# Kernel tuning notes

Hardware: AMD Instinct MI355X
Metric: run time of the kernel (lower is better)

## Reference

```python
import jax, jax.numpy as jnp
import numpy as np


def setup_inputs() -> dict:
    key = jax.random.key(0)
    k1, k2, k3, k4 = jax.random.split(key, 4)
    B, C, L = 16, 512, 4096
    x = jax.random.normal(k1, (B, C, L), dtype=jnp.float32)
    # conv1d kernel_size=1, bias=False -> weight [3C, C]
    w_qkv = jax.random.normal(k2, (3 * C, C), dtype=jnp.float32) * (1.0 / np.sqrt(C))
    w_out = jax.random.normal(k3, (C, C), dtype=jnp.float32) * (1.0 / np.sqrt(C))
    b_out = jax.random.normal(k4, (C,), dtype=jnp.float32) * 0.01
    return {"x": x, "w_qkv": w_qkv, "w_out": w_out, "b_out": b_out}


def reference(x, w_qkv, w_out, b_out):
    # x: [b, c, l]; 1x1 conv == channel-wise matmul
    qkv = jnp.einsum('bcl,oc->bol', x, w_qkv)          # [b, 3c, l]
    q, k, v = jnp.split(qkv, 3, axis=1)                 # each [b, c, l] (heads=1)
    k = jax.nn.softmax(k, axis=-1)                      # softmax over sequence dim l
    context = jnp.einsum('bdn,ben->bde', k, v)          # [b, c, c]
    out = jnp.einsum('bde,bdn->ben', context, q)        # [b, c, l]
    return jnp.einsum('bcl,oc->bol', out, w_out) + b_out[None, :, None]
```

## Files before the change

### kernel.cpp

```cpp
#include <hip/hip_runtime.h>
#include <hip/hip_bf16.h>
#include <type_traits>

#define DEVINL __device__ __forceinline__

typedef float f32x4 __attribute__((ext_vector_type(4)));
typedef __bf16 bf16x8 __attribute__((ext_vector_type(8)));

DEVINL float bf2f(short s) {
  unsigned u = ((unsigned)(unsigned short)s) << 16;
  float f; __builtin_memcpy(&f, &u, 4); return f;
}
DEVINL short f2bf(float f) {
  unsigned u; __builtin_memcpy(&u, &f, 4);
  u += 0x7fff + ((u >> 16) & 1);
  return (short)(u >> 16);
}

DEVINL void gl_lds16(const void* g, void* l) {
  __builtin_amdgcn_global_load_lds(
      (const __attribute__((address_space(1))) void*)g,
      (__attribute__((address_space(3))) void*)l, 16, 0, 0);
}

DEVINL void swz_blk(int& bx, int& by, int& bz) {
  const int gx = gridDim.x, gy = gridDim.y;
  const int tpz = gx * gy;
  const int nwg = tpz * gridDim.z;
  int fid = bx + gx * (by + gy * bz);
  fid = (fid & 7) * (nwg >> 3) + (fid >> 3);
  bz = fid / tpz;
  const int r = fid - bz * tpz;
  by = r % gy;
  bx = r / gy;
}


template <typename OutT, bool BIAS, bool EXP>
DEVINL void epilogue_store(f32x4 (&acc)[4][4], char* smem,
                           OutT* __restrict__ C, int ldc, int m0, int n0,
                           const float* __restrict__ bias,
                           float* __restrict__ rowsum, int t) {
  const int wave = t >> 6, lane = t & 63;
  const int quad = lane >> 4, l16 = lane & 15;
  const int arow = (wave >> 1) * 64, brow = (wave & 1) * 64;
  if constexpr (std::is_same<OutT, float>::value) {
    float* tile = (float*)smem;
#pragma unroll
    for (int rnd = 0; rnd < 2; ++rnd) {
      if ((arow >> 6) == rnd) {
#pragma unroll
        for (int mi = 0; mi < 4; ++mi)
#pragma unroll
          for (int ni = 0; ni < 4; ++ni) {
            const int col = brow + ni * 16 + l16;
#pragma unroll
            for (int r = 0; r < 4; ++r) {
              const int row = mi * 16 + quad * 4 + r;
              float v = acc[mi][ni][r];
              if (BIAS) v += bias[m0 + rnd * 64 + row];
              tile[row * 128 + col] = v;
            }
          }
      }
      __syncthreads();
#pragma unroll
      for (int i = 0; i < 8; ++i) {
        const int row = wave * 16 + i * 2 + (lane >> 5);
        const int cf  = (lane & 31) * 4;
        f32x4 v = *(f32x4*)&tile[row * 128 + cf];
        *(f32x4*)&C[(long)(m0 + rnd * 64 + row) * ldc + n0 + cf] = v;
      }
      __syncthreads();
    }
  } else {
    short* tile = (short*)smem;
#pragma unroll
    for (int mi = 0; mi < 4; ++mi)
#pragma unroll
      for (int r = 0; r < 4; ++r) {
        const int row = arow + mi * 16 + quad * 4 + r;
        float rs = 0.f;
#pragma unroll
        for (int ni = 0; ni < 4; ++ni) {
          const int col = brow + ni * 16 + l16;
          float v = acc[mi][ni][r];
          if (BIAS) v += bias[m0 + row];
          if (EXP) { v = __expf(v); rs += v; }
          tile[row * 128 + col] = f2bf(v);
        }
        if (EXP) {
          rs += __shfl_xor(rs, 1); rs += __shfl_xor(rs, 2);
          rs += __shfl_xor(rs, 4); rs += __shfl_xor(rs, 8);
          if (l16 == 0) atomicAdd(&rowsum[m0 + row], rs);
        }
      }
    __syncthreads();
#pragma unroll
    for (int i = 0; i < 8; ++i) {
      const int row = wave * 32 + i * 4 + (lane >> 4);
      const int cs  = l16 * 8;
      int4 v = *(int4*)&tile[row * 128 + cs];
      *(int4*)&C[(long)(m0 + row) * ldc + n0 + cs] = v;
    }
  }
}

#define GEMM_K_LOOP(A_, lda_, B_, ldb_, kbeg_, kend_)                        \
  {                                                                          \
    const int lrow = t >> 2;                                                 \
    const int lk8  = (t & 3) * 8;                                            \
    auto stage = [&](int buf, int k0) {                                      \
      _Pragma("unroll")                                                      \
      for (int s = 0; s < 2; ++s) {                                          \
        gl_lds16(A_ + (long)(m0 + s * 64 + lrow) * lda_ + k0 + lk8,          \
                 smem + buf * 16384 + s * 4096 + wave * 1024);               \
        gl_lds16(B_ + (long)(n0 + s * 64 + lrow) * ldb_ + k0 + lk8,          \
                 smem + buf * 16384 + 8192 + s * 4096 + wave * 1024);        \
      }                                                                      \
    };                                                                       \
    stage(0, kbeg_);                                                         \
    __syncthreads();                                                         \
    int cur = 0;                                                             \
    for (int k0 = kbeg_; k0 < kend_; k0 += 32) {                             \
      if (k0 + 32 < kend_) stage(cur ^ 1, k0 + 32);                          \
      const short* As = (const short*)(smem + cur * 16384);                  \
      const short* Bs = (const short*)(smem + cur * 16384 + 8192);           \
      bf16x8 af[4], bfr[4];                                                  \
      _Pragma("unroll")                                                      \
      for (int i = 0; i < 4; ++i)                                            \
        af[i] = *(const bf16x8*)&As[(arow + i * 16 + l16) * 32 + quad * 8];  \
      _Pragma("unroll")                                                      \
      for (int i = 0; i < 4; ++i)                                            \
        bfr[i] = *(const bf16x8*)&Bs[(brow + i * 16 + l16) * 32 + quad * 8]; \
      _Pragma("unroll")                                                      \
      for (int mi = 0; mi < 4; ++mi)                                         \
        _Pragma("unroll")                                                    \
        for (int ni = 0; ni < 4; ++ni)                                       \
          acc[mi][ni] = __builtin_amdgcn_mfma_f32_16x16x32_bf16(             \
              af[mi], bfr[ni], acc[mi][ni], 0, 0, 0);                        \
      __syncthreads();                                                       \
      cur ^= 1;                                                              \
    }                                                                        \
  }

template <typename OutT, bool BIAS, bool EXP>
__global__ __launch_bounds__(256, 4)
void gemm_nt(const short* __restrict__ A, long sA, int lda,
             const short* __restrict__ B, long sB, int ldb,
             OutT* __restrict__ C, long sC, int ldc,
             const float* __restrict__ bias, float* __restrict__ rowsum, int K)
{
  int bx = blockIdx.x, by = blockIdx.y, bz = blockIdx.z;
  swz_blk(bx, by, bz);

  A += (long)bz * sA;
  B += (long)bz * sB;
  C += (long)bz * sC;
  if (EXP) rowsum += (long)bz * 512;

  __shared__ char smem[32768];

  const int t    = threadIdx.x;
  const int wave = t >> 6, lane = t & 63;
  const int quad = lane >> 4, l16 = lane & 15;
  const int m0 = by * 128, n0 = bx * 128;
  const int arow = (wave >> 1) * 64, brow = (wave & 1) * 64;

  f32x4 acc[4][4];
#pragma unroll
  for (int i = 0; i < 4; ++i)
#pragma unroll
    for (int j = 0; j < 4; ++j) acc[i][j] = (f32x4){0.f, 0.f, 0.f, 0.f};

  GEMM_K_LOOP(A, lda, B, ldb, 0, K)

  epilogue_store<OutT, BIAS, EXP>(acc, smem, C, ldc, m0, n0, bias, rowsum, t);
}


template <typename OutT, bool BIAS, bool EXP>
DEVINL void epilogue_store_wide(f32x4 (&acc)[4][4], char* smem,
                                OutT* __restrict__ C, int ldc, int m0, int n0,
                                const float* __restrict__ bias,
                                float* __restrict__ rowsum, int t) {
  const int wave = t >> 6, lane = t & 63;
  const int quad = lane >> 4, l16 = lane & 15;
  const int arow = (wave >> 2) * 64, brow = (wave & 3) * 64;
  const int rn_w = brow >> 7;
  const int colb = brow & 64;
  if constexpr (std::is_same<OutT, float>::value) {
    float* tile = (float*)smem;
    const int rm_w = arow >> 6;
#pragma unroll
    for (int rm = 0; rm < 2; ++rm)
#pragma unroll
      for (int rn = 0; rn < 2; ++rn) {
        if (rm_w == rm && rn_w == rn) {
#pragma unroll
          for (int mi = 0; mi < 4; ++mi)
#pragma unroll
            for (int ni = 0; ni < 4; ++ni)
#pragma unroll
              for (int r = 0; r < 4; ++r) {
                const int row = mi * 16 + quad * 4 + r;
                float v = acc[mi][ni][r];
                if (BIAS) v += bias[m0 + rm * 64 + row];
                tile[row * 128 + colb + ni * 16 + l16] = v;
              }
        }
        __syncthreads();
#pragma unroll
        for (int i = 0; i < 4; ++i) {
          const int row = wave * 8 + i * 2 + (lane >> 5);
          const int cf  = (lane & 31) * 4;
          *(f32x4*)&C[(long)(m0 + rm * 64 + row) * ldc + n0 + rn * 128 + cf] =
              *(f32x4*)&tile[row * 128 + cf];
        }
        __syncthreads();
      }
  } else {
    if (EXP) {
#pragma unroll
      for (int mi = 0; mi < 4; ++mi)
#pragma unroll
        for (int r = 0; r < 4; ++r) {
          const int row = arow + mi * 16 + quad * 4 + r;
          float rs = 0.f;
#pragma unroll
          for (int ni = 0; ni < 4; ++ni) {
            float v = __expf(acc[mi][ni][r]);
            acc[mi][ni][r] = v; rs += v;
          }
          rs += __shfl_xor(rs, 1); rs += __shfl_xor(rs, 2);
          rs += __shfl_xor(rs, 4); rs += __shfl_xor(rs, 8);
          if (l16 == 0) atomicAdd(&rowsum[m0 + row], rs);
        }
    }
    short* tile = (short*)smem;
#pragma unroll
    for (int rn = 0; rn < 2; ++rn) {
      if (rn_w == rn) {
#pragma unroll
        for (int mi = 0; mi < 4; ++mi)
#pragma unroll
          for (int ni = 0; ni < 4; ++ni)
#pragma unroll
            for (int r = 0; r < 4; ++r) {
              const int row = arow + mi * 16 + quad * 4 + r;
              float v = acc[mi][ni][r];
              if (BIAS) v += bias[m0 + row];
              tile[row * 128 + colb + ni * 16 + l16] = f2bf(v);
            }
      }
      __syncthreads();
#pragma unroll
      for (int i = 0; i < 4; ++i) {
        const int row = wave * 16 + i * 4 + (lane >> 4);
        const int cs  = l16 * 8;
        *(int4*)&C[(long)(m0 + row) * ldc + n0 + rn * 128 + cs] =
            *(int4*)&tile[row * 128 + cs];
      }
      __syncthreads();
    }
  }
}

#define WIDE_K_LOOP(A_, lda_, B_, ldb_, kbeg_, kend_)                        \
  {                                                                          \
    const int lrow = t >> 2;                                     \
    const int lk8  = (t & 3) * 8;                                            \
    auto stage = [&](int buf, int k0) {                                      \
      gl_lds16(A_ + (long)(m0 + lrow) * lda_ + k0 + lk8,                     \
               smem + buf * 24576 + wave * 1024);                            \
      _Pragma("unroll")                                                      \
      for (int s = 0; s < 2; ++s)                                            \
        gl_lds16(B_ + (long)(n0 + s * 128 + lrow) * ldb_ + k0 + lk8,         \
                 smem + buf * 24576 + 8192 + s * 8192 + wave * 1024);        \
    };                                                                       \
    auto compute = [&](int buf) {                                            \
      const short* As = (const short*)(smem + buf * 24576);                  \
      const short* Bs = (const short*)(smem + buf * 24576 + 8192);           \
      bf16x8 af[4], bfr[4];                                                  \
      _Pragma("unroll")                                                      \
      for (int i = 0; i < 4; ++i)                                            \
        af[i] = *(const bf16x8*)&As[(arow + i * 16 + l16) * 32 + quad * 8];  \
      _Pragma("unroll")                                                      \
      for (int i = 0; i < 4; ++i)                                            \
        bfr[i] = *(const bf16x8*)&Bs[(brow + i * 16 + l16) * 32 + quad * 8]; \
      _Pragma("unroll")                                                      \
      for (int mi = 0; mi < 4; ++mi)                                         \
        _Pragma("unroll")                                                    \
        for (int ni = 0; ni < 4; ++ni)                                       \
          acc[mi][ni] = __builtin_amdgcn_mfma_f32_16x16x32_bf16(             \
              af[mi], bfr[ni], acc[mi][ni], 0, 0, 0);                        \
    };                                                                       \
    stage(0, kbeg_);                                                         \
    stage(1, kbeg_ + 32);                                                    \
    int cur = 0;                                                             \
    for (int k0 = kbeg_; k0 < kend_ - 32; k0 += 32) {                        \
      asm volatile("s_waitcnt vmcnt(3)" ::: "memory");                       \
      __builtin_amdgcn_s_barrier();                                          \
      __builtin_amdgcn_sched_barrier(0);                                     \
      if (k0 + 64 < kend_) {                                                 \
        int nb = cur + 2; if (nb >= 3) nb -= 3;                              \
        stage(nb, k0 + 64);                                                  \
      }                                                                      \
      compute(cur);                                                          \
      ++cur; if (cur == 3) cur = 0;                                          \
    }                                                                        \
    asm volatile("s_waitcnt vmcnt(0)" ::: "memory");                         \
    __builtin_amdgcn_s_barrier();                                            \
    __builtin_amdgcn_sched_barrier(0);                                       \
    compute(cur);                                                            \
    __syncthreads();                        \
  }

template <typename OutT, bool BIAS, bool EXP>
__global__ __launch_bounds__(512, 4)
void gemm_nt_wide(const short* __restrict__ A, long sA, int lda,
                  const short* __restrict__ B, long sB, int ldb,
                  OutT* __restrict__ C, long sC, int ldc,
                  const float* __restrict__ bias, float* __restrict__ rowsum,
                  int K)
{
  int bx = blockIdx.x, by = blockIdx.y, bz = blockIdx.z;
  swz_blk(bx, by, bz);

  A += (long)bz * sA;
  B += (long)bz * sB;
  C += (long)bz * sC;
  if (EXP) rowsum += (long)bz * 512;

  __shared__ char smem[73728];

  const int t    = threadIdx.x;
  const int wave = t >> 6, lane = t & 63;
  const int quad = lane >> 4, l16 = lane & 15;
  const int m0 = by * 128, n0 = bx * 256;
  const int arow = (wave >> 2) * 64, brow = (wave & 3) * 64;

  f32x4 acc[4][4];
#pragma unroll
  for (int i = 0; i < 4; ++i)
#pragma unroll
    for (int j = 0; j < 4; ++j) acc[i][j] = (f32x4){0.f, 0.f, 0.f, 0.f};

  WIDE_K_LOOP(A, lda, B, ldb, 0, K)

  epilogue_store_wide<OutT, BIAS, EXP>(acc, smem, C, ldc, m0, n0, bias,
                                       rowsum, t);
}

__global__ __launch_bounds__(512, 4)
void gemm_sk_wide(const short* __restrict__ Ab, const short* __restrict__ Bb,
                  float* __restrict__ Cp)
{
  int bx = blockIdx.x, by = blockIdx.y, bz = blockIdx.z;
  swz_blk(bx, by, bz);

  const int b = bz >> 1, s = bz & 1;
  const short* A = Ab + (long)b * 2097152;
  const short* B = Bb + (long)b * 2097152;
  float* C = Cp + (long)(s * 16 + b) * 262144;

  __shared__ char smem[73728];

  const int t    = threadIdx.x;
  const int wave = t >> 6, lane = t & 63;
  const int quad = lane >> 4, l16 = lane & 15;
  const int m0 = by * 128, n0 = bx * 256;
  const int arow = (wave >> 2) * 64, brow = (wave & 3) * 64;
  const int kbeg = s * 2048, kend = kbeg + 2048;

  f32x4 acc[4][4];
#pragma unroll
  for (int i = 0; i < 4; ++i)
#pragma unroll
    for (int j = 0; j < 4; ++j) acc[i][j] = (f32x4){0.f, 0.f, 0.f, 0.f};

  WIDE_K_LOOP(A, 4096, B, 4096, kbeg, kend)

  epilogue_store_wide<float, false, false>(acc, smem, C, 512, m0, n0, nullptr,
                                           nullptr, t);
}

__global__ void reduce_sk(const float* __restrict__ p, short* __restrict__ o,
                          const float* __restrict__ s) {
  const long i = ((long)blockIdx.x * 256 + threadIdx.x) * 4;
  const float inv = 1.f / s[i >> 9];
  f32x4 a = *(const f32x4*)&p[i];
  f32x4 b = *(const f32x4*)&p[i + 4194304];
  short r[4];
#pragma unroll
  for (int j = 0; j < 4; ++j) r[j] = f2bf((a[j] + b[j]) * inv);
  *(long*)&o[i] = *(long*)r;
}


__global__ void cast_bf16(const float* __restrict__ x, short* __restrict__ xb) {
  const long stride = (long)gridDim.x * 256 * 8;
  for (long i = ((long)blockIdx.x * 256 + threadIdx.x) * 8; i < 33554432;
       i += stride) {
    f32x4 a = *(const f32x4*)&x[i];
    f32x4 b = *(const f32x4*)&x[i + 4];
    short r[8];
#pragma unroll
    for (int j = 0; j < 4; ++j) r[j] = f2bf(a[j]);
#pragma unroll
    for (int j = 0; j < 4; ++j) r[4 + j] = f2bf(b[j]);
    *(int4*)&xb[i] = *(int4*)r;
  }
}

__global__ void transpose8(const short* __restrict__ xb,
                           short* __restrict__ xT) {
  const long g = (long)blockIdx.x * 256 + threadIdx.x;
  const int c8 = (int)(g & 63);
  const int l8 = (int)((g >> 6) & 511);
  const int b  = (int)(g >> 15);
  const short* src = xb + ((long)b << 21) + (long)(c8 * 8) * 4096 + l8 * 8;
  short s[8][8];
#pragma unroll
  for (int i = 0; i < 8; ++i)
    *(int4*)s[i] = *(const int4*)(src + (long)i * 4096);
  short* dst = xT + ((long)b << 21) + (long)(l8 * 8) * 512 + c8 * 8;
#pragma unroll
  for (int j = 0; j < 8; ++j) {
    short o[8];
#pragma unroll
    for (int i = 0; i < 8; ++i) o[i] = s[i][j];
    *(int4*)(dst + (long)j * 512) = *(int4*)o;
  }
}

DEVINL float to_f(float v) { return v; }
DEVINL float to_f(short v) { return bf2f(v); }

template <typename InT, typename OutT>
__global__ void transpose_k(const InT* __restrict__ src, OutT* __restrict__ dst,
                            int R, int Cc, long ss, long ds)
{
  __shared__ float tile[32][33];
  src += (long)blockIdx.z * ss;
  dst += (long)blockIdx.z * ds;
  const int c0 = blockIdx.x * 32, r0 = blockIdx.y * 32;
  const int tx = threadIdx.x, ty = threadIdx.y;
#pragma unroll
  for (int i = 0; i < 4; ++i)
    tile[ty + i * 8][tx] = to_f(src[(long)(r0 + ty + i * 8) * Cc + c0 + tx]);
  __syncthreads();
#pragma unroll
  for (int i = 0; i < 4; ++i) {
    float v = tile[tx][ty + i * 8];
    if constexpr (std::is_same<OutT, float>::value)
      dst[(long)(c0 + ty + i * 8) * R + r0 + tx] = v;
    else
      dst[(long)(c0 + ty + i * 8) * R + r0 + tx] = f2bf(v);
  }
}

__global__ void cast_weights(const float* __restrict__ wq, short* __restrict__ wqb,
                             const float* __restrict__ wo, short* __restrict__ wob,
                             float* __restrict__ ssum) {
  const int i = blockIdx.x * 256 + threadIdx.x;
  if (blockIdx.x < 32) ssum[i] = 0.f;
  if (i < 786432) wqb[i] = f2bf(wq[i]);
  else            wob[i - 786432] = f2bf(wo[i - 786432]);
}

extern "C" void kernel_launch(void* const* d_in, const int* in_sizes, int n_in,
                              void* d_out, int out_size, void* d_ws, size_t ws_size,
                              hipStream_t stream) {
  const float* x     = (const float*)d_in[0];
  const float* w_qkv = (const float*)d_in[1];
  const float* w_out = (const float*)d_in[2];
  const float* b_out = (const float*)d_in[3];
  float* out = (float*)d_out;

  const long CL = (long)512 * 4096;
  const long CC = (long)512 * 512;

  char* ws = (char*)d_ws;
  short* xT  = (short*)(ws);
  short* xb  = (short*)(ws + 67108864);
  short* kbf = (short*)(ws + 134217728);
  float* Pp  = (float*)(ws + 201326592);
  short* P   = (short*)(ws + 268435456);
  short* U   = (short*)(ws + 276824064);
  short* wvT = (short*)(ws + 277348352);
  short* M2  = (short*)(ws + 285212672);
  short* M3  = (short*)(ws + 293601280);
  short* wqb = (short*)(ws + 301989888);
  short* wob = (short*)(ws + 303562752);
  short* wqT = (short*)(ws + 304087040);
  float* ssum = (float*)(ws + 293601280);

  cast_weights<<<4096, 256, 0, stream>>>(w_qkv, wqb, w_out, wob, ssum);

  transpose_k<float, short><<<dim3(16, 16, 1), dim3(32, 8), 0, stream>>>(
      w_qkv, wqT, 512, 512, 0, 0);
  transpose_k<short, short><<<dim3(16, 16, 1), dim3(32, 8), 0, stream>>>(
      wqb + 2 * CC, wvT, 512, 512, 0, 0);

  gemm_nt<short, false, false><<<dim3(4, 4, 1), 256, 0, stream>>>(
      wob, 0, 512, wvT, 0, 512, U, 0, 512, nullptr, nullptr, 512);

  cast_bf16<<<2048, 256, 0, stream>>>(x, xb);
  transpose8<<<2048, 256, 0, stream>>>(xb, xT);

  gemm_nt_wide<short, false, true><<<dim3(16, 4, 16), 512, 0, stream>>>(
      wqb + CC, 0, 512, xT, CL, 512, kbf, CL, 4096, nullptr, ssum, 512);

  gemm_sk_wide<<<dim3(2, 4, 32), 512, 0, stream>>>(kbf, xb, Pp);
  reduce_sk<<<4096, 256, 0, stream>>>(Pp, P, ssum);

  gemm_nt<short, false, false><<<dim3(4, 4, 16), 256, 0, stream>>>(
      U, 0, 512, P, CC, 512, M2, CC, 512, nullptr, nullptr, 512);

  gemm_nt<short, false, false><<<dim3(4, 4, 16), 256, 0, stream>>>(
      M2, CC, 512, wqT, 0, 512, M3, CC, 512, nullptr, nullptr, 512);

  gemm_nt_wide<float, true, false><<<dim3(16, 4, 16), 512, 0, stream>>>(
      M3, CC, 512, xT, CL, 512, out, CL, 4096, b_out, nullptr, 512);
}
```

Measured before the change: 469.7 us.

## Fuse x cast with transpose, merge weight prep, deepen split-K pipeline

Combines the fp32→bf16 cast of x and its transpose into one kernel that reads x once and writes both layouts, removing a full re-read of the bf16 copy. Merges weight casting and the two weight transposes into a single launch. Gives the split-K GEMM a 4-buffer load pipeline with more LDS and a lower occupancy hint, trading occupancy for deeper prefetch.

After: 499.6 us. +6.4%, slower.

```diff
diff --git a/kernel.cpp b/kernel.cpp
--- a/kernel.cpp
+++ b/kernel.cpp
@@ -266,21 +266,20 @@
   }
 }
 
-#define WIDE_K_LOOP(A_, lda_, B_, ldb_, kbeg_, kend_)                        \
-  {                                                                          \
+#define WIDE_STAGE_COMPUTE(A_, lda_, B_, ldb_, BUFSZ_)                       \
     const int lrow = t >> 2;                                     \
     const int lk8  = (t & 3) * 8;                                            \
     auto stage = [&](int buf, int k0) {                                      \
       gl_lds16(A_ + (long)(m0 + lrow) * lda_ + k0 + lk8,                     \
-               smem + buf * 24576 + wave * 1024);                            \
+               smem + buf * BUFSZ_ + wave * 1024);                           \
       _Pragma("unroll")                                                      \
       for (int s = 0; s < 2; ++s)                                            \
         gl_lds16(B_ + (long)(n0 + s * 128 + lrow) * ldb_ + k0 + lk8,         \
-                 smem + buf * 24576 + 8192 + s * 8192 + wave * 1024);        \
+                 smem + buf * BUFSZ_ + 8192 + s * 8192 + wave * 1024);       \
     };                                                                       \
     auto compute = [&](int buf) {                                            \
-      const short* As = (const short*)(smem + buf * 24576);                  \
-      const short* Bs = (const short*)(smem + buf * 24576 + 8192);           \
+      const short* As = (const short*)(smem + buf * BUFSZ_);                 \
+      const short* Bs = (const short*)(smem + buf * BUFSZ_ + 8192);          \
       bf16x8 af[4], bfr[4];                                                  \
       _Pragma("unroll")                                                      \
       for (int i = 0; i < 4; ++i)                                            \
@@ -294,7 +293,11 @@
         for (int ni = 0; ni < 4; ++ni)                                       \
           acc[mi][ni] = __builtin_amdgcn_mfma_f32_16x16x32_bf16(             \
               af[mi], bfr[ni], acc[mi][ni], 0, 0, 0);                        \
-    };                                                                       \
+    };
+
+#define WIDE_K_LOOP(A_, lda_, B_, ldb_, kbeg_, kend_)                        \
+  {                                                                          \
+    WIDE_STAGE_COMPUTE(A_, lda_, B_, ldb_, 24576)                            \
     stage(0, kbeg_);                                                         \
     stage(1, kbeg_ + 32);                                                    \
     int cur = 0;                                                             \
@@ -316,6 +319,27 @@
     __syncthreads();                        \
   }
 
+#define WIDE4_K_LOOP(A_, lda_, B_, ldb_, kbeg_, kend_)                       \
+  {                                                                          \
+    WIDE_STAGE_COMPUTE(A_, lda_, B_, ldb_, 24576)                            \
+    stage(0, kbeg_);                                                         \
+    stage(1, kbeg_ + 32);                                                    \
+    stage(2, kbeg_ + 64);                                                    \
+    int cur = 0;                                                             \
+    for (int k0 = kbeg_; k0 < kend_; k0 += 32) {                             \
+      const int rem = kend_ - k0;                                            \
+      if (rem >= 96)      asm volatile("s_waitcnt vmcnt(6)" ::: "memory");   \
+      else if (rem == 64) asm volatile("s_waitcnt vmcnt(3)" ::: "memory");   \
+      else                asm volatile("s_waitcnt vmcnt(0)" ::: "memory");   \
+      __builtin_amdgcn_s_barrier();                                          \
+      __builtin_amdgcn_sched_barrier(0);                                     \
+      if (rem > 96) stage((cur + 3) & 3, k0 + 96);                           \
+      compute(cur);                                                          \
+      cur = (cur + 1) & 3;                                                   \
+    }                                                                        \
+    __syncthreads();                        \
+  }
+
 template <typename OutT, bool BIAS, bool EXP>
 __global__ __launch_bounds__(512, 4)
 void gemm_nt_wide(const short* __restrict__ A, long sA, int lda,
@@ -352,7 +376,7 @@
                                        rowsum, t);
 }
 
-__global__ __launch_bounds__(512, 4)
+__global__ __launch_bounds__(512, 2)
 void gemm_sk_wide(const short* __restrict__ Ab, const short* __restrict__ Bb,
                   float* __restrict__ Cp)
 {
@@ -364,7 +388,7 @@
   const short* B = Bb + (long)b * 2097152;
   float* C = Cp + (long)(s * 16 + b) * 262144;
 
-  __shared__ char smem[73728];
+  __shared__ char smem[98304];
 
   const int t    = threadIdx.x;
   const int wave = t >> 6, lane = t & 63;
@@ -379,7 +403,7 @@
 #pragma unroll
     for (int j = 0; j < 4; ++j) acc[i][j] = (f32x4){0.f, 0.f, 0.f, 0.f};
 
-  WIDE_K_LOOP(A, 4096, B, 4096, kbeg, kend)
+  WIDE4_K_LOOP(A, 4096, B, 4096, kbeg, kend)
 
   epilogue_store_wide<float, false, false>(acc, smem, C, 512, m0, n0, nullptr,
                                            nullptr, t);
@@ -397,76 +421,72 @@
   *(long*)&o[i] = *(long*)r;
 }
 
-
-__global__ void cast_bf16(const float* __restrict__ x, short* __restrict__ xb) {
-  const long stride = (long)gridDim.x * 256 * 8;
-  for (long i = ((long)blockIdx.x * 256 + threadIdx.x) * 8; i < 33554432;
-       i += stride) {
-    f32x4 a = *(const f32x4*)&x[i];
-    f32x4 b = *(const f32x4*)&x[i + 4];
-    short r[8];
-#pragma unroll
-    for (int j = 0; j < 4; ++j) r[j] = f2bf(a[j]);
-#pragma unroll
-    for (int j = 0; j < 4; ++j) r[4 + j] = f2bf(b[j]);
-    *(int4*)&xb[i] = *(int4*)r;
-  }
-}
-
-__global__ void transpose8(const short* __restrict__ xb,
-                           short* __restrict__ xT) {
+__global__ void prep_x(const float* __restrict__ x, short* __restrict__ xb,
+                       short* __restrict__ xT) {
   const long g = (long)blockIdx.x * 256 + threadIdx.x;
   const int c8 = (int)(g & 63);
   const int l8 = (int)((g >> 6) & 511);
   const int b  = (int)(g >> 15);
-  const short* src = xb + ((long)b << 21) + (long)(c8 * 8) * 4096 + l8 * 8;
+  const float* src = x + ((long)b << 21) + (long)(c8 * 8) * 4096 + l8 * 8;
+
+  f32x4 lo[8], hi[8];
+#pragma unroll
+  for (int i = 0; i < 8; ++i) {
+    lo[i] = *(const f32x4*)(src + (long)i * 4096);
+    hi[i] = *(const f32x4*)(src + (long)i * 4096 + 4);
+  }
+  __builtin_amdgcn_sched_barrier(0);
+
   short s[8][8];
 #pragma unroll
   for (int i = 0; i < 8; ++i)
-    *(int4*)s[i] = *(const int4*)(src + (long)i * 4096);
-  short* dst = xT + ((long)b << 21) + (long)(l8 * 8) * 512 + c8 * 8;
+#pragma unroll
+    for (int j = 0; j < 4; ++j) {
+      s[i][j]     = f2bf(lo[i][j]);
+      s[i][4 + j] = f2bf(hi[i][j]);
+    }
+
+  short* db = xb + ((long)b << 21) + (long)(c8 * 8) * 4096 + l8 * 8;
+#pragma unroll
+  for (int i = 0; i < 8; ++i)
+    *(int4*)(db + (long)i * 4096) = *(int4*)s[i];
+
+  short* dt = xT + ((long)b << 21) + (long)(l8 * 8) * 512 + c8 * 8;
 #pragma unroll
   for (int j = 0; j < 8; ++j) {
     short o[8];
 #pragma unroll
     for (int i = 0; i < 8; ++i) o[i] = s[i][j];
-    *(int4*)(dst + (long)j * 512) = *(int4*)o;
-  }
-}
-
-DEVINL float to_f(float v) { return v; }
-DEVINL float to_f(short v) { return bf2f(v); }
-
-template <typename InT, typename OutT>
-__global__ void transpose_k(const InT* __restrict__ src, OutT* __restrict__ dst,
-                            int R, int Cc, long ss, long ds)
-{
+    *(int4*)(dt + (long)j * 512) = *(int4*)o;
+  }
+}
+
+__global__ void prep_w(const float* __restrict__ wq, short* __restrict__ wqb,
+                       const float* __restrict__ wo, short* __restrict__ wob,
+                       float* __restrict__ ssum, short* __restrict__ wqT,
+                       short* __restrict__ wvT) {
   __shared__ float tile[32][33];
-  src += (long)blockIdx.z * ss;
-  dst += (long)blockIdx.z * ds;
-  const int c0 = blockIdx.x * 32, r0 = blockIdx.y * 32;
-  const int tx = threadIdx.x, ty = threadIdx.y;
-#pragma unroll
-  for (int i = 0; i < 4; ++i)
-    tile[ty + i * 8][tx] = to_f(src[(long)(r0 + ty + i * 8) * Cc + c0 + tx]);
-  __syncthreads();
-#pragma unroll
-  for (int i = 0; i < 4; ++i) {
-    float v = tile[tx][ty + i * 8];
-    if constexpr (std::is_same<OutT, float>::value)
-      dst[(long)(c0 + ty + i * 8) * R + r0 + tx] = v;
-    else
-      dst[(long)(c0 + ty + i * 8) * R + r0 + tx] = f2bf(v);
-  }
-}
-
-__global__ void cast_weights(const float* __restrict__ wq, short* __restrict__ wqb,
-                             const float* __restrict__ wo, short* __restrict__ wob,
-                             float* __restrict__ ssum) {
-  const int i = blockIdx.x * 256 + threadIdx.x;
-  if (blockIdx.x < 32) ssum[i] = 0.f;
-  if (i < 786432) wqb[i] = f2bf(wq[i]);
-  else            wob[i - 786432] = f2bf(wo[i - 786432]);
+  const int blk = blockIdx.x, t = threadIdx.x;
+  if (blk < 4096) {
+    const int i = blk * 256 + t;
+    if (blk < 32) ssum[i] = 0.f;
+    if (i < 786432) wqb[i] = f2bf(wq[i]);
+    else            wob[i - 786432] = f2bf(wo[i - 786432]);
+  } else {
+    const int s = blk - 4096;
+    const float* src = (s >> 8) ? wq + 524288 : wq;
+    short* dst = (s >> 8) ? wvT : wqT;
+    const int b2 = s & 255;
+    const int c0 = (b2 & 15) * 32, r0 = (b2 >> 4) * 32;
+    const int tx = t & 31, ty = t >> 5;
+#pragma unroll
+    for (int i = 0; i < 4; ++i)
+      tile[ty + i * 8][tx] = src[(r0 + ty + i * 8) * 512 + c0 + tx];
+    __syncthreads();
+#pragma unroll
+    for (int i = 0; i < 4; ++i)
+      dst[(c0 + ty + i * 8) * 512 + r0 + tx] = f2bf(tile[tx][ty + i * 8]);
+  }
 }
 
 extern "C" void kernel_launch(void* const* d_in, const int* in_sizes, int n_in,
@@ -496,18 +516,12 @@
   short* wqT = (short*)(ws + 304087040);
   float* ssum = (float*)(ws + 293601280);
 
-  cast_weights<<<4096, 256, 0, stream>>>(w_qkv, wqb, w_out, wob, ssum);
-
-  transpose_k<float, short><<<dim3(16, 16, 1), dim3(32, 8), 0, stream>>>(
-      w_qkv, wqT, 512, 512, 0, 0);
-  transpose_k<short, short><<<dim3(16, 16, 1), dim3(32, 8), 0, stream>>>(
-      wqb + 2 * CC, wvT, 512, 512, 0, 0);
+  prep_w<<<4608, 256, 0, stream>>>(w_qkv, wqb, w_out, wob, ssum, wqT, wvT);
 
   gemm_nt<short, false, false><<<dim3(4, 4, 1), 256, 0, stream>>>(
       wob, 0, 512, wvT, 0, 512, U, 0, 512, nullptr, nullptr, 512);
 
-  cast_bf16<<<2048, 256, 0, stream>>>(x, xb);
-  transpose8<<<2048, 256, 0, stream>>>(xb, xT);
+  prep_x<<<2048, 256, 0, stream>>>(x, xb, xT);
 
   gemm_nt_wide<short, false, true><<<dim3(16, 4, 16), 512, 0, stream>>>(
       wqb + CC, 0, 512, xT, CL, 512, kbf, CL, 4096, nullptr, ssum, 512);
```
